# Kernel optimization log

Measured on AMD Instinct MI355X. Metric: run time of the kernel, lower is better.

## Reference

```python
import jax, jax.numpy as jnp
import numpy as np
from jax import lax

PERM = (0, 1, 4, 5, 2, 3)  # swap the two (H,W) spatial pairs
DN = ('NCHWXY', 'OIHWXY', 'NCHWXY')  # 4 spatial dims -> native 4D conv


def conv4d(x, w, b):
    # x: [B,Ci,S,S,S,S], w: [Co,Ci,k1,k1,k2,k2], 'SAME' padding as in ANCNet Conv4d
    y = lax.conv_general_dilated(x, w, window_strides=(1, 1, 1, 1),
                                 padding='SAME', dimension_numbers=DN)
    return y + b[None, :, None, None, None, None]


def setup_inputs() -> dict:
    key = jax.random.key(0)
    ks = jax.random.split(key, 10)
    B, S = 2, 25
    def w_init(k, shape):
        fan_in = shape[1] * np.prod(shape[2:])
        return jax.random.normal(k, shape, jnp.float32) * (1.0 / np.sqrt(fan_in))
    return {
        'x': jax.random.normal(ks[0], (B, 1, S, S, S, S), jnp.float32),
        'w0': w_init(ks[1], (8, 1, 3, 3, 5, 5)),   'b0': jnp.zeros((8,), jnp.float32),
        'w1': w_init(ks[2], (8, 1, 5, 5, 5, 5)),   'b1': jnp.zeros((8,), jnp.float32),
        'w2a': w_init(ks[3], (16, 16, 5, 5, 5, 5)), 'b2a': jnp.zeros((16,), jnp.float32),
        'w2b': w_init(ks[4], (1, 16, 5, 5, 5, 5)),  'b2b': jnp.zeros((1,), jnp.float32),
    }


def reference(x, w0, b0, w1, b1, w2a, b2a, w2b, b2b):
    relu = jax.nn.relu
    conv0 = lambda t: relu(conv4d(t, w0, b0))
    conv1 = lambda t: relu(conv4d(t, w1, b1))
    conv2 = lambda t: relu(conv4d(relu(conv4d(t, w2a, b2a)), w2b, b2b))
    sym = lambda f, t: f(t) + jnp.transpose(f(jnp.transpose(t, PERM)), PERM)
    x0 = sym(conv0, x)
    x1 = sym(conv1, x)
    h = jnp.concatenate((x0, x1), axis=1)  # [B,16,S,S,S,S]
    return sym(conv2, h)
```

## Files before the change

### kernel.cpp

```cpp
#include <hip/hip_runtime.h>

#define S 25
#define PLANE 625
#define VOL 390625
#define CLn 12500000
#define HREG 6728
#define LDSPAD 20224

typedef __attribute__((ext_vector_type(8))) short short8;
typedef __attribute__((ext_vector_type(4))) float f32x4;
typedef __attribute__((ext_vector_type(16))) float f32x16;
typedef __attribute__((ext_vector_type(4))) unsigned short us4;
typedef __attribute__((ext_vector_type(4))) unsigned int u32x4;

__device__ __forceinline__ unsigned short f2bf(float f) {
    unsigned int u = __float_as_uint(f);
    u += 0x7fffu + ((u >> 16) & 1u);
    return (unsigned short)(u >> 16);
}

__device__ __forceinline__ int xcd_swz(int orig, int nwg) {
    int q = nwg >> 3, r = nwg & 7;
    int x = orig & 7, lid = orig >> 3;
    return (x < r ? x * (q + 1) : r * (q + 1) + (x - r) * q) + lid;
}

__device__ __forceinline__ int nxt_kd(int kd, int d0, int d1) {
    #pragma unroll 1
    for (++kd; kd < 25; ++kd) {
        int kd0 = kd / 5, kd1 = kd - kd0 * 5;
        int e0 = d0 + kd0 - 2, e1 = d1 + kd1 - 2;
        if (e0 >= 0 && e0 < S && e1 >= 0 && e1 < S) return kd;
    }
    return 25;
}

__device__ __forceinline__ int nxt_w(int uv, int U, int V, int b0, int b1) {
    #pragma unroll 1
    for (++uv; uv < U * V; ++uv) {
        int u = uv / V, v = uv - u * V;
        int e0 = b0 + u, e1 = b1 + v;
        if (e0 >= 0 && e0 < S && e1 >= 0 && e1 < S) return uv;
    }
    return U * V;
}

__global__ __launch_bounds__(256) void prep_weights(
    const float* __restrict__ w2a, const float* __restrict__ w2b,
    const float* __restrict__ w0, const float* __restrict__ w1,
    unsigned short* __restrict__ wbig32, unsigned short* __restrict__ wl1,
    unsigned short* __restrict__ wcp)
{
    int idx = blockIdx.x * 256 + threadIdx.x;
    if (idx < 320000) {
        int k = idx & 15;
        int m = (idx >> 4) & 31;
        int rem = idx >> 9;
        int t = rem % 25, kd01 = rem / 25;
        float v;
        if (m < 16) v = w2a[(m * 16 + k) * 625 + kd01 * 25 + t];
        else        v = w2a[((m - 16) * 16 + k) * 625 + t * 25 + kd01];
        wbig32[idx] = f2bf(v);
    } else if (idx < 345600) {
        int j = idx - 320000;
        int k = j & 31;
        int row = (j >> 5) & 15;
        int tile = (j >> 9) & 1;
        int kd01 = j >> 10;
        int kd0 = kd01 / 5, kd1 = kd01 - kd0 * 5;
        float v = 0.f;
        if (k < 25) {
            int t = k, kd2 = t / 5, kd3 = t - kd2 * 5;
            if (tile == 0) {
                v = (row < 8) ? w1[row * 625 + kd0 * 125 + kd1 * 25 + t]
                              : w1[(row - 8) * 625 + t * 25 + kd01];
            } else {
                if (row < 8) {
                    if (kd0 >= 1 && kd0 <= 3 && kd1 >= 1 && kd1 <= 3)
                        v = w0[((row * 3 + (kd0 - 1)) * 3 + (kd1 - 1)) * 25 + t];
                } else {
                    if (kd2 >= 1 && kd2 <= 3 && kd3 >= 1 && kd3 <= 3)
                        v = w0[(row - 8) * 225 + ((kd2 - 1) * 3 + (kd3 - 1)) * 25 + kd01];
                }
            }
        }
        wl1[j] = f2bf(v);
    } else if (idx < 345600 + 614400) {
        int j = idx - 345600;
        int k = j & 31;
        int row = (j >> 5) & 15;
        int rem = j >> 9;
        int t = rem % 25, uv = rem / 25;
        int u = uv >> 3, v8 = uv & 7;
        int path = row & 1, o = row >> 1;
        int py = o >> 2, px = o & 3;
        int kd0 = u - py, kd1 = v8 - px;
        float v = 0.f;
        if (kd0 >= 0 && kd0 < 5 && kd1 >= 0 && kd1 < 5) {
            int ci = k & 15;
            if (path == 0 && k < 16)
                v = w2b[ci * 625 + (kd0 * 5 + kd1) * 25 + t];
            else if (path == 1 && k >= 16)
                v = w2b[ci * 625 + t * 25 + kd0 * 5 + kd1];
        }
        wcp[j] = f2bf(v);
    }
}

__global__ __launch_bounds__(256) void layer1_mfma(
    const float* __restrict__ x, const unsigned short* __restrict__ wl1,
    const float* __restrict__ b0, const float* __restrict__ b1,
    unsigned short* __restrict__ hbf)
{
    __shared__ __align__(16) unsigned short pl[29 * 32];
    const int blk = blockIdx.x;
    const int b = blk / PLANE;
    const int d01 = blk - b * PLANE;
    const int d0 = d01 / S, d1 = d01 - d0 * S;
    const int tid = threadIdx.x;
    const int l = tid & 63, w = tid >> 6;
    const int col = l & 15, kq = l >> 4;

    int off[8];
    #pragma unroll
    for (int j = 0; j < 8; ++j) {
        int t = kq * 8 + j; if (t > 24) t = 24;
        int t5 = t / 5;
        off[j] = t5 * 32 + (t - t5 * 5);
    }
    int rb[10];
    #pragma unroll
    for (int g = 0; g < 10; ++g) {
        int n = (w * 10 + g) * 16 + col; if (n > 624) n = 624;
        int d2 = n / 25;
        rb[g] = d2 * 32 + (n - d2 * 25);
    }

    f32x4 acc0[10], acc1[10];
    #pragma unroll
    for (int g = 0; g < 10; ++g) {
        acc0[g] = (f32x4){0.f, 0.f, 0.f, 0.f};
        acc1[g] = (f32x4){0.f, 0.f, 0.f, 0.f};
    }

    const float* xb = x + (size_t)b * VOL;

    #pragma unroll 1
    for (int kd01 = 0; kd01 < 25; ++kd01) {
        const int kd0 = kd01 / 5, kd1 = kd01 - kd0 * 5;
        const int e0 = d0 + kd0 - 2, e1 = d1 + kd1 - 2;
        if (e0 < 0 || e0 >= S || e1 < 0 || e1 >= S) continue;
        __syncthreads();
        {
            const float* sp = xb + (e0 * 25 + e1) * 625;
            for (int i = tid; i < 841; i += 256) {
                int r = i / 29, c = i - r * 29;
                float v = 0.f;
                if (r >= 2 && r <= 26 && c >= 2 && c <= 26)
                    v = sp[(r - 2) * 25 + (c - 2)];
                pl[r * 32 + c] = f2bf(v);
            }
        }
        __syncthreads();
        const unsigned short* wp = wl1 + kd01 * 1024;
        short8 a0 = *(const short8*)(wp + col * 32 + kq * 8);
        short8 a1 = *(const short8*)(wp + 512 + col * 32 + kq * 8);
        #pragma unroll
        for (int g = 0; g < 10; ++g) {
            short8 bf;
            #pragma unroll
            for (int j = 0; j < 8; ++j)
                bf[j] = (short)pl[rb[g] + off[j]];
            acc0[g] = __builtin_amdgcn_mfma_f32_16x16x32_bf16(a0, bf, acc0[g], 0, 0, 0);
            acc1[g] = __builtin_amdgcn_mfma_f32_16x16x32_bf16(a1, bf, acc1[g], 0, 0, 0);
        }
    }

    const int ch = (kq & 1) * 4;
    float bi1[4], bi0[4];
    #pragma unroll
    for (int r = 0; r < 4; ++r) { bi1[r] = b1[ch + r]; bi0[r] = b0[ch + r]; }
    const bool lo = (kq < 2);
    const size_t obase = (size_t)(b * 625 + d01) * 625;
    #pragma unroll
    for (int g = 0; g < 10; ++g) {
        int n = (w * 10 + g) * 16 + col;
        float r0[4], r1[4];
        #pragma unroll
        for (int r = 0; r < 4; ++r) {
            r0[r] = fmaxf(acc0[g][r] + bi1[r], 0.f);
            r1[r] = fmaxf(acc1[g][r] + bi0[r], 0.f);
        }
        us4 u0, u1;
        #pragma unroll
        for (int r = 0; r < 4; ++r) {
            float p0 = __shfl_xor(r0[r], 32, 64);
            float p1 = __shfl_xor(r1[r], 32, 64);
            u0[r] = f2bf(r0[r] + p0);
            u1[r] = f2bf(r1[r] + p1);
        }
        if (lo && n < 625) {
            *(us4*)&hbf[(obase + n) * 16 + 8 + ch] = u0;
            *(us4*)&hbf[(obase + n) * 16 + ch]     = u1;
        }
    }
}

__global__ __launch_bounds__(256, 3) void conv_mfma32(
    const unsigned short* __restrict__ in, const unsigned short* __restrict__ wq,
    const float* __restrict__ bias,
    unsigned short* __restrict__ gA, unsigned short* __restrict__ gB)
{
    __shared__ __align__(16) unsigned short pl[LDSPAD];
    const int blk = xcd_swz(blockIdx.x, 1250);
    const int b = blk / PLANE;
    const int d01 = blk - b * PLANE;
    const int d0 = d01 / S, d1 = d01 - d0 * S;
    const int tid = threadIdx.x;
    const int l = tid & 63, w = tid >> 6;
    const int h = l >> 5;
    const int nl = l & 31;

    int ofsG[7], ofsL[7]; bool ok[7];
    #pragma unroll
    for (int j = 0; j < 7; ++j) {
        int cid = tid + j * 256;
        int hh = (cid >= 841) ? 1 : 0;
        int pt = cid - hh * 841;
        int r = pt / 29, c = pt - r * 29;
        ok[j] = (cid < 1682) && (r >= 2 && r <= 26 && c >= 2 && c <= 26);
        ofsG[j] = ((r - 2) * 25 + (c - 2)) * 16 + hh * 8;
        ofsL[j] = hh * HREG + pt * 8;
    }

    int rbo[5];
    #pragma unroll
    for (int g = 0; g < 5; ++g) {
        int n = (w * 5 + g) * 32 + nl;
        if (n > 624) n = 624;
        int d2 = n / 25, d3 = n - d2 * 25;
        rbo[g] = h * HREG + (d2 * 29 + d3) * 8;
    }

    f32x16 acc[5];
    #pragma unroll
    for (int g = 0; g < 5; ++g)
        #pragma unroll
        for (int r = 0; r < 16; ++r) acc[g][r] = 0.f;

    const unsigned short* inb = in + (size_t)b * 6250000;

    u32x4 stg[7];
    int kd_cur = nxt_kd(-1, d0, d1);
    {
        int kd0 = kd_cur / 5, kd1 = kd_cur - kd0 * 5;
        const unsigned short* sb = inb + (size_t)((d0 + kd0 - 2) * 25 + (d1 + kd1 - 2)) * 10000;
        #pragma unroll
        for (int j = 0; j < 7; ++j) {
            u32x4 z = {0u, 0u, 0u, 0u};
            if (ok[j]) z = *(const u32x4*)(sb + ofsG[j]);
            stg[j] = z;
        }
    }

    #pragma unroll 1
    while (kd_cur < 25) {
        const int kd01 = kd_cur;
        const int kd_nxt = nxt_kd(kd_cur, d0, d1);
        __syncthreads();
        #pragma unroll
        for (int j = 0; j < 7; ++j)
            if (j < 6 || tid < 146) *(u32x4*)&pl[ofsL[j]] = stg[j];
        __syncthreads();
        if (kd_nxt < 25) {
            int kd0 = kd_nxt / 5, kd1 = kd_nxt - kd0 * 5;
            const unsigned short* sb = inb + (size_t)((d0 + kd0 - 2) * 25 + (d1 + kd1 - 2)) * 10000;
            #pragma unroll
            for (int j = 0; j < 7; ++j) {
                u32x4 z = {0u, 0u, 0u, 0u};
                if (ok[j]) z = *(const u32x4*)(sb + ofsG[j]);
                stg[j] = z;
            }
        }

        const unsigned short* wkd = wq + (size_t)kd01 * 25 * 512 + nl * 16 + h * 8;
        #pragma unroll 1
        for (int t = 0; t < 25; ++t) {
            short8 a = *(const short8*)(wkd + t * 512);
            int t5 = t / 5;
            int toff = (t5 * 29 + (t - t5 * 5)) * 8;
            #pragma unroll
            for (int g = 0; g < 5; ++g) {
                short8 bf = *(const short8*)&pl[rbo[g] + toff];
                acc[g] = __builtin_amdgcn_mfma_f32_32x32x16_bf16(a, bf, acc[g], 0, 0, 0);
            }
        }
        kd_cur = kd_nxt;
    }

    #pragma unroll
    for (int g = 0; g < 5; ++g) {
        int n = (w * 5 + g) * 32 + nl;
        if (n < 625) {
            size_t ob = ((size_t)(b * 625 + d01) * 625 + n) * 16;
            #pragma unroll
            for (int q = 0; q < 4; ++q) {
                int baserow = q * 8 + 4 * h;
                us4 u;
                #pragma unroll
                for (int r = 0; r < 4; ++r) {
                    int co = (baserow + r) & 15;
                    u[r] = f2bf(fmaxf(acc[g][q * 4 + r] + bias[co], 0.f));
                }
                if (baserow < 16) *(us4*)&gA[ob + baserow] = u;
                else              *(us4*)&gB[ob + baserow - 16] = u;
            }
        }
    }
}

__global__ __launch_bounds__(128, 2) void convc_v3(
    const unsigned short* __restrict__ gA,
    const unsigned short* __restrict__ wcp, const float* __restrict__ b2b,
    float* __restrict__ outp)
{
    __shared__ __align__(16) unsigned short pl[348 * 36];
    const int blk = xcd_swz(blockIdx.x, 728);
    const int q = blk & 3;
    const int geo = blk >> 2;
    const int b = geo / 91;
    const int g91 = geo - b * 91;
    const int t0 = g91 / 7, t1 = g91 - t0 * 7;
    const int D0 = t0 * 2, D1 = t1 * 4;
    const int r0 = (q == 0) ? -2 : (q == 1) ? 4 : (q == 2) ? 10 : 17;
    const int tid = threadIdx.x;
    const int l = tid & 63, w = tid >> 6;
    const int col = l & 15, kq = l >> 4;

    int ofsG[11], ofsL[11]; bool ok[11];
    #pragma unroll
    for (int j = 0; j < 11; ++j) {
        int cid = tid + j * 128;
        int p = cid >> 2, qq = cid & 3;
        int r = p / 29, c = p - r * 29;
        int d2e = r + r0, d3e = c - 2;
        ok[j] = (cid < 1392) && (d2e >= 0 && d2e < S) && (d3e >= 0 && d3e < S);
        ofsG[j] = (qq >> 1) * CLn + (d2e * 25 + d3e) * 16 + (qq & 1) * 8;
        ofsL[j] = p * 36 + qq * 8;
    }

    int rb[5];
    #pragma unroll
    for (int g = 0; g < 5; ++g) {
        int n = q * 160 + (w * 5 + g) * 16 + col; if (n > 624) n = 624;
        int d2 = n / 25;
        rb[g] = ((d2 - r0 - 2) * 29 + (n - d2 * 25)) * 36;
    }

    f32x4 acc[5];
    #pragma unroll
    for (int g = 0; g < 5; ++g) acc[g] = (f32x4){0.f, 0.f, 0.f, 0.f};

    const unsigned short* gAb = gA + (size_t)b * 6250000;

    u32x4 stg[11];
    int uv_cur = nxt_w(-1, 6, 8, D0 - 2, D1 - 2);
    {
        int u = uv_cur >> 3, v = uv_cur & 7;
        const unsigned short* sb = gAb + (size_t)((D0 - 2 + u) * 25 + (D1 - 2 + v)) * 10000;
        #pragma unroll
        for (int j = 0; j < 11; ++j) {
            u32x4 z = {0u, 0u, 0u, 0u};
            if (ok[j]) z = *(const u32x4*)(sb + ofsG[j]);
            stg[j] = z;
        }
    }

    #pragma unroll 1
    while (uv_cur < 48) {
        const int uvc = uv_cur;
        const int uv_nxt = nxt_w(uv_cur, 6, 8, D0 - 2, D1 - 2);
        __syncthreads();
        #pragma unroll
        for (int j = 0; j < 11; ++j)
            if (j < 10 || tid < 112) *(u32x4*)&pl[ofsL[j]] = stg[j];
        __syncthreads();
        if (uv_nxt < 48) {
            int u = uv_nxt >> 3, v = uv_nxt & 7;
            const unsigned short* sb = gAb + (size_t)((D0 - 2 + u) * 25 + (D1 - 2 + v)) * 10000;
            #pragma unroll
            for (int j = 0; j < 11; ++j) {
                u32x4 z = {0u, 0u, 0u, 0u};
                if (ok[j]) z = *(const u32x4*)(sb + ofsG[j]);
                stg[j] = z;
            }
        }

        const unsigned short* wbase = wcp + (size_t)uvc * 12800;
        #pragma unroll 1
        for (int t = 0; t < 25; ++t) {
            const int t5 = t / 5;
            const int toff = (t5 * 29 + (t - t5 * 5)) * 36;
            short8 a = *(const short8*)(wbase + (t * 16 + col) * 32 + kq * 8);
            #pragma unroll
            for (int g = 0; g < 5; ++g) {
                short8 bf = *(const short8*)&pl[rb[g] + toff + kq * 8];
                acc[g] = __builtin_amdgcn_mfma_f32_16x16x32_bf16(a, bf, acc[g], 0, 0, 0);
            }
        }
        uv_cur = uv_nxt;
    }

    const float bv = b2b[0];
    #pragma unroll
    for (int g = 0; g < 5; ++g) {
        int n = q * 160 + (w * 5 + g) * 16 + col;
        if (n < 625) {
            #pragma unroll
            for (int r2 = 0; r2 < 2; ++r2) {
                int o = kq * 2 + r2;
                int d0 = D0 + (o >> 2), d1 = D1 + (o & 3);
                if (d0 < S && d1 < S) {
                    float vA = acc[g][r2 * 2], vB = acc[g][r2 * 2 + 1];
                    outp[((size_t)b * 625 + d0 * 25 + d1) * 625 + n] =
                        fmaxf(vA + bv, 0.f) + fmaxf(vB + bv, 0.f);
                }
            }
        }
    }
}

extern "C" void kernel_launch(void* const* d_in, const int* in_sizes, int n_in,
                              void* d_out, int out_size, void* d_ws, size_t ws_size,
                              hipStream_t stream) {
    const float* x   = (const float*)d_in[0];
    const float* w0  = (const float*)d_in[1];
    const float* b0  = (const float*)d_in[2];
    const float* w1  = (const float*)d_in[3];
    const float* b1  = (const float*)d_in[4];
    const float* w2a = (const float*)d_in[5];
    const float* b2a = (const float*)d_in[6];
    const float* w2b = (const float*)d_in[7];
    const float* b2b = (const float*)d_in[8];
    float* out = (float*)d_out;

    unsigned short* hbf    = (unsigned short*)d_ws;
    unsigned short* gA     = hbf + CLn;
    unsigned short* gB     = gA + CLn;
    unsigned short* wbig32 = gB + CLn;
    unsigned short* wl1    = wbig32 + 320000;
    unsigned short* wcp    = wl1 + 25600;
    if (ws_size < ((size_t)3 * CLn + 320000 + 25600 + 614400) * sizeof(unsigned short)) return;

    prep_weights<<<3750, 256, 0, stream>>>(w2a, w2b, w0, w1, wbig32, wl1, wcp);
    layer1_mfma<<<1250, 256, 0, stream>>>(x, wl1, b0, b1, hbf);
    conv_mfma32<<<1250, 256, 0, stream>>>(hbf, wbig32, b2a, gA, gB);
    convc_v3<<<728, 128, 0, stream>>>(gA, wcp, b2b, out);
}
```

Measured before the change: 953.1 us.

## Compute two adjacent output d1 positions per block to reuse staged input planes

The main 4D conv kernel now assigns each block two neighbouring d1 output positions. It iterates over a 5x6 window of input planes, and each staged LDS plane feeds MFMAs into two accumulator sets using shifted weight taps. This cuts the number of global-to-LDS plane loads per output from 25 to about 15, and it halves the grid. In exchange the accumulator register count doubles, occupancy drops to 2 blocks per CU, and fewer blocks (650) are available to fill the device.

```diff
diff --git a/kernel.cpp b/kernel.cpp
--- a/kernel.cpp
+++ b/kernel.cpp
@@ -23,16 +23,6 @@
     int q = nwg >> 3, r = nwg & 7;
     int x = orig & 7, lid = orig >> 3;
     return (x < r ? x * (q + 1) : r * (q + 1) + (x - r) * q) + lid;
-}
-
-__device__ __forceinline__ int nxt_kd(int kd, int d0, int d1) {
-    #pragma unroll 1
-    for (++kd; kd < 25; ++kd) {
-        int kd0 = kd / 5, kd1 = kd - kd0 * 5;
-        int e0 = d0 + kd0 - 2, e1 = d1 + kd1 - 2;
-        if (e0 >= 0 && e0 < S && e1 >= 0 && e1 < S) return kd;
-    }
-    return 25;
 }
 
 __device__ __forceinline__ int nxt_w(int uv, int U, int V, int b0, int b1) {
@@ -206,16 +196,18 @@
     }
 }
 
-__global__ __launch_bounds__(256, 3) void conv_mfma32(
+__global__ __launch_bounds__(256, 2) void conv_mfma32p2(
     const unsigned short* __restrict__ in, const unsigned short* __restrict__ wq,
     const float* __restrict__ bias,
     unsigned short* __restrict__ gA, unsigned short* __restrict__ gB)
 {
     __shared__ __align__(16) unsigned short pl[LDSPAD];
-    const int blk = xcd_swz(blockIdx.x, 1250);
-    const int b = blk / PLANE;
-    const int d01 = blk - b * PLANE;
-    const int d0 = d01 / S, d1 = d01 - d0 * S;
+    const int blk = xcd_swz(blockIdx.x, 650);
+    const int b = blk / 325;
+    const int rem = blk - b * 325;
+    const int d0 = rem / 13, dp = rem - d0 * 13;
+    const int d1a = dp * 2;
+    const bool haveB = (d1a + 1 < S);
     const int tid = threadIdx.x;
     const int l = tid & 63, w = tid >> 6;
     const int h = l >> 5;
@@ -242,19 +234,19 @@
         rbo[g] = h * HREG + (d2 * 29 + d3) * 8;
     }
 
-    f32x16 acc[5];
+    f32x16 acc0[5], acc1[5];
     #pragma unroll
     for (int g = 0; g < 5; ++g)
         #pragma unroll
-        for (int r = 0; r < 16; ++r) acc[g][r] = 0.f;
+        for (int r = 0; r < 16; ++r) { acc0[g][r] = 0.f; acc1[g][r] = 0.f; }
 
     const unsigned short* inb = in + (size_t)b * 6250000;
 
     u32x4 stg[7];
-    int kd_cur = nxt_kd(-1, d0, d1);
+    int uv_cur = nxt_w(-1, 5, 6, d0 - 2, d1a - 2);
     {
-        int kd0 = kd_cur / 5, kd1 = kd_cur - kd0 * 5;
-        const unsigned short* sb = inb + (size_t)((d0 + kd0 - 2) * 25 + (d1 + kd1 - 2)) * 10000;
+        int u = uv_cur / 6, v = uv_cur - u * 6;
+        const unsigned short* sb = inb + (size_t)((d0 + u - 2) * 25 + (d1a + v - 2)) * 10000;
         #pragma unroll
         for (int j = 0; j < 7; ++j) {
             u32x4 z = {0u, 0u, 0u, 0u};
@@ -264,17 +256,17 @@
     }
 
     #pragma unroll 1
-    while (kd_cur < 25) {
-        const int kd01 = kd_cur;
-        const int kd_nxt = nxt_kd(kd_cur, d0, d1);
+    while (uv_cur < 30) {
+        const int u = uv_cur / 6, v = uv_cur - u * 6;
+        const int uv_nxt = nxt_w(uv_cur, 5, 6, d0 - 2, d1a - 2);
         __syncthreads();
         #pragma unroll
         for (int j = 0; j < 7; ++j)
             if (j < 6 || tid < 146) *(u32x4*)&pl[ofsL[j]] = stg[j];
         __syncthreads();
-        if (kd_nxt < 25) {
-            int kd0 = kd_nxt / 5, kd1 = kd_nxt - kd0 * 5;
-            const unsigned short* sb = inb + (size_t)((d0 + kd0 - 2) * 25 + (d1 + kd1 - 2)) * 10000;
+        if (uv_nxt < 30) {
+            int un = uv_nxt / 6, vn = uv_nxt - un * 6;
+            const unsigned short* sb = inb + (size_t)((d0 + un - 2) * 25 + (d1a + vn - 2)) * 10000;
             #pragma unroll
             for (int j = 0; j < 7; ++j) {
                 u32x4 z = {0u, 0u, 0u, 0u};
@@ -283,37 +275,57 @@
             }
         }
 
-        const unsigned short* wkd = wq + (size_t)kd01 * 25 * 512 + nl * 16 + h * 8;
+        const bool vp0 = (v < 5);
+        const bool vp1 = (v >= 1) && haveB;
+        const unsigned short* wkd0 = wq + (size_t)(vp0 ? (u * 5 + v) : 0) * 12800 + nl * 16 + h * 8;
+        const unsigned short* wkd1 = wq + (size_t)(vp1 ? (u * 5 + v - 1) : 0) * 12800 + nl * 16 + h * 8;
+
         #pragma unroll 1
         for (int t = 0; t < 25; ++t) {
-            short8 a = *(const short8*)(wkd + t * 512);
-            int t5 = t / 5;
-            int toff = (t5 * 29 + (t - t5 * 5)) * 8;
-            #pragma unroll
-            for (int g = 0; g < 5; ++g) {
-                short8 bf = *(const short8*)&pl[rbo[g] + toff];
-                acc[g] = __builtin_amdgcn_mfma_f32_32x32x16_bf16(a, bf, acc[g], 0, 0, 0);
-            }
-        }
-        kd_cur = kd_nxt;
-    }
-
-    #pragma unroll
-    for (int g = 0; g < 5; ++g) {
-        int n = (w * 5 + g) * 32 + nl;
-        if (n < 625) {
-            size_t ob = ((size_t)(b * 625 + d01) * 625 + n) * 16;
-            #pragma unroll
-            for (int q = 0; q < 4; ++q) {
-                int baserow = q * 8 + 4 * h;
-                us4 u;
+            const int t5 = t / 5;
+            const int toff = (t5 * 29 + (t - t5 * 5)) * 8;
+            short8 bf[5];
+            #pragma unroll
+            for (int g = 0; g < 5; ++g)
+                bf[g] = *(const short8*)&pl[rbo[g] + toff];
+            if (vp0) {
+                short8 a = *(const short8*)(wkd0 + t * 512);
                 #pragma unroll
-                for (int r = 0; r < 4; ++r) {
-                    int co = (baserow + r) & 15;
-                    u[r] = f2bf(fmaxf(acc[g][q * 4 + r] + bias[co], 0.f));
+                for (int g = 0; g < 5; ++g)
+                    acc0[g] = __builtin_amdgcn_mfma_f32_32x32x16_bf16(a, bf[g], acc0[g], 0, 0, 0);
+            }
+            if (vp1) {
+                short8 a = *(const short8*)(wkd1 + t * 512);
+                #pragma unroll
+                for (int g = 0; g < 5; ++g)
+                    acc1[g] = __builtin_amdgcn_mfma_f32_32x32x16_bf16(a, bf[g], acc1[g], 0, 0, 0);
+            }
+        }
+        uv_cur = uv_nxt;
+    }
+
+    #pragma unroll
+    for (int p = 0; p < 2; ++p) {
+        if (p == 1 && !haveB) break;
+        const size_t obase = ((size_t)b * 625 + d0 * 25 + d1a + p) * 625;
+        #pragma unroll
+        for (int g = 0; g < 5; ++g) {
+            int n = (w * 5 + g) * 32 + nl;
+            if (n < 625) {
+                size_t ob = (obase + n) * 16;
+                #pragma unroll
+                for (int q = 0; q < 4; ++q) {
+                    int baserow = q * 8 + 4 * h;
+                    us4 u;
+                    #pragma unroll
+                    for (int r = 0; r < 4; ++r) {
+                        int co = (baserow + r) & 15;
+                        float av = p ? acc1[g][q * 4 + r] : acc0[g][q * 4 + r];
+                        u[r] = f2bf(fmaxf(av + bias[co], 0.f));
+                    }
+                    if (baserow < 16) *(us4*)&gA[ob + baserow] = u;
+                    else              *(us4*)&gB[ob + baserow - 16] = u;
                 }
-                if (baserow < 16) *(us4*)&gA[ob + baserow] = u;
-                else              *(us4*)&gB[ob + baserow - 16] = u;
             }
         }
     }
@@ -454,6 +466,6 @@
 
     prep_weights<<<3750, 256, 0, stream>>>(w2a, w2b, w0, w1, wbig32, wl1, wcp);
     layer1_mfma<<<1250, 256, 0, stream>>>(x, wl1, b0, b1, hbf);
-    conv_mfma32<<<1250, 256, 0, stream>>>(hbf, wbig32, b2a, gA, gB);
+    conv_mfma32p2<<<650, 256, 0, stream>>>(hbf, wbig32, b2a, gA, gB);
     convc_v3<<<728, 128, 0, stream>>>(gA, wcp, b2b, out);
 }
```

Measured after the change: 1.123 ms. 17.8% more time.

## Stage conv input planes directly into LDS with global_load_lds

Applied to the files above, without the earlier changes.

Replaces register-staged prefetch (global load into VGPRs, then ds_write) in conv_mfma32 with direct global-to-LDS loads via __builtin_amdgcn_global_load_lds. A small zeroed workspace buffer supplies the padding halo, and the LDS layout is remapped to a per-wave contiguous one with a new half-plane stride. This removes the VGPR staging array and the LDS write instructions. In exchange, the next plane is now loaded only after the MFMA loop finishes on a single buffer, so load latency is no longer overlapped with compute inside a block and relies on other resident blocks to hide it.

```diff
diff --git a/kernel.cpp b/kernel.cpp
--- a/kernel.cpp
+++ b/kernel.cpp
@@ -4,7 +4,7 @@
 #define PLANE 625
 #define VOL 390625
 #define CLn 12500000
-#define HREG 6728
+#define HREG2 7168
 #define LDSPAD 20224
 
 typedef __attribute__((ext_vector_type(8))) short short8;
@@ -17,6 +17,12 @@
     unsigned int u = __float_as_uint(f);
     u += 0x7fffu + ((u >> 16) & 1u);
     return (unsigned short)(u >> 16);
+}
+
+__device__ __forceinline__ void glds16(const unsigned short* g, unsigned short* l) {
+    __builtin_amdgcn_global_load_lds(
+        (const __attribute__((address_space(1))) unsigned int*)g,
+        (__attribute__((address_space(3))) unsigned int*)l, 16, 0, 0);
 }
 
 __device__ __forceinline__ int xcd_swz(int orig, int nwg) {
@@ -49,7 +55,7 @@
     const float* __restrict__ w2a, const float* __restrict__ w2b,
     const float* __restrict__ w0, const float* __restrict__ w1,
     unsigned short* __restrict__ wbig32, unsigned short* __restrict__ wl1,
-    unsigned short* __restrict__ wcp)
+    unsigned short* __restrict__ wcp, unsigned short* __restrict__ z16)
 {
     int idx = blockIdx.x * 256 + threadIdx.x;
     if (idx < 320000) {
@@ -104,6 +110,8 @@
                 v = w2b[ci * 625 + t * 25 + kd0 * 5 + kd1];
         }
         wcp[j] = f2bf(v);
+    } else if (idx < 345600 + 614400 + 8) {
+        z16[idx - 960000] = 0;
     }
 }
 
@@ -208,7 +216,7 @@
 
 __global__ __launch_bounds__(256, 3) void conv_mfma32(
     const unsigned short* __restrict__ in, const unsigned short* __restrict__ wq,
-    const float* __restrict__ bias,
+    const float* __restrict__ bias, const unsigned short* __restrict__ z16,
     unsigned short* __restrict__ gA, unsigned short* __restrict__ gB)
 {
     __shared__ __align__(16) unsigned short pl[LDSPAD];
@@ -221,16 +229,15 @@
     const int h = l >> 5;
     const int nl = l & 31;
 
-    int ofsG[7], ofsL[7]; bool ok[7];
+    int srcofs[7]; bool okz[7];
     #pragma unroll
     for (int j = 0; j < 7; ++j) {
-        int cid = tid + j * 256;
-        int hh = (cid >= 841) ? 1 : 0;
-        int pt = cid - hh * 841;
+        int cid = (j * 4 + w) * 64 + l;
+        int half = (cid >= 896) ? 1 : 0;
+        int pt = cid - half * 896;
         int r = pt / 29, c = pt - r * 29;
-        ok[j] = (cid < 1682) && (r >= 2 && r <= 26 && c >= 2 && c <= 26);
-        ofsG[j] = ((r - 2) * 25 + (c - 2)) * 16 + hh * 8;
-        ofsL[j] = hh * HREG + pt * 8;
+        okz[j] = (pt < 841) && (r >= 2 && r <= 26 && c >= 2 && c <= 26);
+        srcofs[j] = ((r - 2) * 25 + (c - 2)) * 16 + half * 8;
     }
 
     int rbo[5];
@@ -239,7 +246,7 @@
         int n = (w * 5 + g) * 32 + nl;
         if (n > 624) n = 624;
         int d2 = n / 25, d3 = n - d2 * 25;
-        rbo[g] = h * HREG + (d2 * 29 + d3) * 8;
+        rbo[g] = h * HREG2 + (d2 * 29 + d3) * 8;
     }
 
     f32x16 acc[5];
@@ -250,17 +257,13 @@
 
     const unsigned short* inb = in + (size_t)b * 6250000;
 
-    u32x4 stg[7];
     int kd_cur = nxt_kd(-1, d0, d1);
     {
         int kd0 = kd_cur / 5, kd1 = kd_cur - kd0 * 5;
         const unsigned short* sb = inb + (size_t)((d0 + kd0 - 2) * 25 + (d1 + kd1 - 2)) * 10000;
         #pragma unroll
-        for (int j = 0; j < 7; ++j) {
-            u32x4 z = {0u, 0u, 0u, 0u};
-            if (ok[j]) z = *(const u32x4*)(sb + ofsG[j]);
-            stg[j] = z;
-        }
+        for (int j = 0; j < 7; ++j)
+            glds16(okz[j] ? sb + srcofs[j] : z16, &pl[(j * 4 + w) * 512]);
     }
 
     #pragma unroll 1
@@ -268,22 +271,8 @@
         const int kd01 = kd_cur;
         const int kd_nxt = nxt_kd(kd_cur, d0, d1);
         __syncthreads();
-        #pragma unroll
-        for (int j = 0; j < 7; ++j)
-            if (j < 6 || tid < 146) *(u32x4*)&pl[ofsL[j]] = stg[j];
-        __syncthreads();
-        if (kd_nxt < 25) {
-            int kd0 = kd_nxt / 5, kd1 = kd_nxt - kd0 * 5;
-            const unsigned short* sb = inb + (size_t)((d0 + kd0 - 2) * 25 + (d1 + kd1 - 2)) * 10000;
-            #pragma unroll
-            for (int j = 0; j < 7; ++j) {
-                u32x4 z = {0u, 0u, 0u, 0u};
-                if (ok[j]) z = *(const u32x4*)(sb + ofsG[j]);
-                stg[j] = z;
-            }
-        }
-
-        const unsigned short* wkd = wq + (size_t)kd01 * 25 * 512 + nl * 16 + h * 8;
+
+        const unsigned short* wkd = wq + (size_t)kd01 * 12800 + nl * 16 + h * 8;
         #pragma unroll 1
         for (int t = 0; t < 25; ++t) {
             short8 a = *(const short8*)(wkd + t * 512);
@@ -294,6 +283,15 @@
                 short8 bf = *(const short8*)&pl[rbo[g] + toff];
                 acc[g] = __builtin_amdgcn_mfma_f32_32x32x16_bf16(a, bf, acc[g], 0, 0, 0);
             }
+        }
+
+        __syncthreads();
+        if (kd_nxt < 25) {
+            int kd0 = kd_nxt / 5, kd1 = kd_nxt - kd0 * 5;
+            const unsigned short* sb = inb + (size_t)((d0 + kd0 - 2) * 25 + (d1 + kd1 - 2)) * 10000;
+            #pragma unroll
+            for (int j = 0; j < 7; ++j)
+                glds16(okz[j] ? sb + srcofs[j] : z16, &pl[(j * 4 + w) * 512]);
         }
         kd_cur = kd_nxt;
     }
@@ -450,10 +448,11 @@
     unsigned short* wbig32 = gB + CLn;
     unsigned short* wl1    = wbig32 + 320000;
     unsigned short* wcp    = wl1 + 25600;
-    if (ws_size < ((size_t)3 * CLn + 320000 + 25600 + 614400) * sizeof(unsigned short)) return;
-
-    prep_weights<<<3750, 256, 0, stream>>>(w2a, w2b, w0, w1, wbig32, wl1, wcp);
+    unsigned short* z16    = wcp + 614400;
+    if (ws_size < ((size_t)3 * CLn + 320000 + 25600 + 614400 + 8) * sizeof(unsigned short)) return;
+
+    prep_weights<<<3751, 256, 0, stream>>>(w2a, w2b, w0, w1, wbig32, wl1, wcp, z16);
     layer1_mfma<<<1250, 256, 0, stream>>>(x, wl1, b0, b1, hbf);
-    conv_mfma32<<<1250, 256, 0, stream>>>(hbf, wbig32, b2a, gA, gB);
+    conv_mfma32<<<1250, 256, 0, stream>>>(hbf, wbig32, b2a, z16, gA, gB);
     convc_v3<<<728, 128, 0, stream>>>(gA, wcp, b2b, out);
 }
```

Measured after the change: 959.9 us. Within noise of the previous version (+0.7%).
